# Kernel tuning notes

Hardware: AMD Instinct MI355X
Metric: run time of the kernel (lower is better)

## Reference

```python
import jax, jax.numpy as jnp
import numpy as np

B = 500000
DT = 1.0

def _first_principles_A(dt):
    A = np.eye(8, dtype=np.float32)
    for i in range(4):
        A[i, i + 4] = dt
    return jnp.asarray(A)

def setup_inputs() -> dict:
    key = jax.random.key(0)
    k1, k2 = jax.random.split(key)
    # bbox-like state: keep positions/sizes positive so Q heuristic is sensible
    x = jax.random.uniform(k1, (B, 8, 1), dtype=jnp.float32, minval=0.1, maxval=1.0)
    P = jax.random.normal(k2, (B, 8, 8), dtype=jnp.float32) * 0.1
    A = _first_principles_A(DT)  # relu/triu leave it unchanged but we apply them anyway
    sigma_p = jnp.float32(0.05)
    sigma_v = jnp.float32(0.00625)
    return {"x": x, "P": P, "A": A, "sigma_p": sigma_p, "sigma_v": sigma_v}

def reference(x, P, A, sigma_p, sigma_v):
    # get_motion_matrix: relu then triu
    Ap = jnp.triu(jax.nn.relu(A))  # (8, 8)
    # x_hat = A @ x
    x_hat = jnp.einsum('ij,bjk->bik', Ap, x)  # (B, 8, 1)
    # process-noise heuristic: diag proportional to bbox h, w (x[:,2,0], x[:,3,0])
    h = x[:, 2, 0]
    w = x[:, 3, 0]
    xp, yp = h * sigma_p, w * sigma_p
    xv, yv = h * sigma_v, w * sigma_v
    diag = jnp.stack([xp, yp, xp, yp, xv, yv, xv, yv], axis=-1)  # (B, 8)
    Q = jnp.square(diag)[:, :, None] * jnp.eye(8, dtype=x.dtype)  # (B, 8, 8) diagonal
    # P_hat = A P A^T + Q
    P_hat = jnp.einsum('ij,bjk,lk->bil', Ap, P, Ap) + Q
    return (x_hat, P_hat)
```

## Files before the change

### kernel.cpp

```cpp
#include <hip/hip_runtime.h>


#define ROW_STRIDE 12
#define ELEM_STRIDE 100
#define ELEMS_PER_BLOCK 32

__global__ __launch_bounds__(256) void kalman_predict_kernel(
    const float* __restrict__ x,
    const float* __restrict__ P,
    const float* __restrict__ A,
    const float* __restrict__ sigp_ptr,
    const float* __restrict__ sigv_ptr,
    float* __restrict__ x_hat,
    float* __restrict__ P_hat,
    int B)
{
    __shared__ float lds_m[ELEMS_PER_BLOCK * ELEM_STRIDE];

    float ap[64];
#pragma unroll
    for (int t = 0; t < 64; ++t) {
        float a = fmaxf(A[t], 0.0f);
        if ((t & 7) < (t >> 3)) a = 0.0f;
        ap[t] = __int_as_float(__builtin_amdgcn_readfirstlane(__float_as_int(a)));
    }
    float sigma_p = __int_as_float(__builtin_amdgcn_readfirstlane(__float_as_int(sigp_ptr[0])));
    float sigma_v = __int_as_float(__builtin_amdgcn_readfirstlane(__float_as_int(sigv_ptr[0])));

    int tid = blockIdx.x * blockDim.x + threadIdx.x;
    int e = tid >> 3;
    int r = tid & 7;
    int e_l = threadIdx.x >> 3;

    bool valid = (e < B);
    int e_c = valid ? e : (B - 1);

    const float4* prow = (const float4*)(P + (size_t)e_c * 64 + r * 8);
    float4 pa = prow[0], pb = prow[1];
    float p[8] = {pa.x, pa.y, pa.z, pa.w, pb.x, pb.y, pb.z, pb.w};

    const float4* xrow = (const float4*)(x + (size_t)e_c * 8);
    float4 x0 = xrow[0], x1 = xrow[1];
    float xv[8] = {x0.x, x0.y, x0.z, x0.w, x1.x, x1.y, x1.z, x1.w};

    const float4* arow = (const float4*)(A + r * 8);
    float4 a0 = arow[0], a1 = arow[1];
    float apr[8] = {a0.x, a0.y, a0.z, a0.w, a1.x, a1.y, a1.z, a1.w};
#pragma unroll
    for (int j = 0; j < 8; ++j) {
        float v = fmaxf(apr[j], 0.0f);
        apr[j] = (j >= r) ? v : 0.0f;
    }

    float m[8];
#pragma unroll
    for (int l = 0; l < 8; ++l) {
        float s = 0.0f;
#pragma unroll
        for (int k = 0; k < 8; ++k) s = fmaf(ap[l * 8 + k], p[k], s);
        m[l] = s;
    }

    float* slot = lds_m + e_l * ELEM_STRIDE + r * ROW_STRIDE;
    ((float4*)slot)[0] = make_float4(m[0], m[1], m[2], m[3]);
    ((float4*)(slot + 4))[0] = make_float4(m[4], m[5], m[6], m[7]);

    __syncthreads();

    float hv = (r & 1) ? xv[3] : xv[2];
    float sig = (r < 4) ? sigma_p : sigma_v;
    float q = hv * sig;
    q = q * q;

    float xh = 0.0f;
#pragma unroll
    for (int j = 0; j < 8; ++j) xh = fmaf(apr[j], xv[j], xh);

    float out[8];
#pragma unroll
    for (int l = 0; l < 8; ++l) out[l] = (l == r) ? q : 0.0f;

    const float* ebase = lds_m + e_l * ELEM_STRIDE;
#pragma unroll
    for (int j = 0; j < 8; ++j) {
        const float4* mr = (const float4*)(ebase + j * ROW_STRIDE);
        float4 ma = mr[0], mb = mr[1];
        float mj[8] = {ma.x, ma.y, ma.z, ma.w, mb.x, mb.y, mb.z, mb.w};
#pragma unroll
        for (int l = 0; l < 8; ++l) out[l] = fmaf(apr[j], mj[l], out[l]);
    }

    if (valid) {
        x_hat[(size_t)e * 8 + r] = xh;
        float4* po = (float4*)(P_hat + (size_t)e * 64 + r * 8);
        po[0] = make_float4(out[0], out[1], out[2], out[3]);
        po[1] = make_float4(out[4], out[5], out[6], out[7]);
    }
}

extern "C" void kernel_launch(void* const* d_in, const int* in_sizes, int n_in,
                              void* d_out, int out_size, void* d_ws, size_t ws_size,
                              hipStream_t stream) {
    const float* x  = (const float*)d_in[0];
    const float* P  = (const float*)d_in[1];
    const float* A  = (const float*)d_in[2];
    const float* sp = (const float*)d_in[3];
    const float* sv = (const float*)d_in[4];

    int B = in_sizes[0] / 8;
    float* x_hat = (float*)d_out;
    float* P_hat = (float*)d_out + (size_t)B * 8;

    int threads = B * 8;
    int block = 256;
    int grid = (threads + block - 1) / block;
    kalman_predict_kernel<<<grid, block, 0, stream>>>(x, P, A, sp, sv, x_hat, P_hat, B);
}
```

Before: 253.5 us.

## Precompute masked A in setup kernel, drop block barrier, skip triangular zeros

Adds a tiny setup kernel that applies relu/triu to A and stores it plus sigma values in a global constant buffer, removing per-thread preprocessing from the main kernel. Replaces __syncthreads with a wave-local LDS wait, relying on the 8 threads of each element being in the same wavefront. Skips multiplications by the structurally zero lower triangle and uses 32-bit index arithmetic. Adds a second kernel launch and relies on wavefront-local synchronization assumptions.

Measured after the change: 251.7 us. Within noise of the previous version (-0.7%).

```diff
diff --git a/kernel.cpp b/kernel.cpp
--- a/kernel.cpp
+++ b/kernel.cpp
@@ -5,27 +5,29 @@
 #define ELEM_STRIDE 100
 #define ELEMS_PER_BLOCK 32
 
+__device__ __align__(16) float g_cst[72];
+
+__global__ void kalman_setup_kernel(const float* __restrict__ A,
+                                    const float* __restrict__ sigp_ptr,
+                                    const float* __restrict__ sigv_ptr)
+{
+    int t = threadIdx.x;
+    if (t < 64) {
+        float a = fmaxf(A[t], 0.0f);
+        if ((t & 7) < (t >> 3)) a = 0.0f;
+        g_cst[t] = a;
+    }
+    if (t < 8) g_cst[64 + t] = (t < 4) ? sigp_ptr[0] : sigv_ptr[0];
+}
+
 __global__ __launch_bounds__(256) void kalman_predict_kernel(
     const float* __restrict__ x,
     const float* __restrict__ P,
-    const float* __restrict__ A,
-    const float* __restrict__ sigp_ptr,
-    const float* __restrict__ sigv_ptr,
     float* __restrict__ x_hat,
     float* __restrict__ P_hat,
     int B)
 {
     __shared__ float lds_m[ELEMS_PER_BLOCK * ELEM_STRIDE];
-
-    float ap[64];
-#pragma unroll
-    for (int t = 0; t < 64; ++t) {
-        float a = fmaxf(A[t], 0.0f);
-        if ((t & 7) < (t >> 3)) a = 0.0f;
-        ap[t] = __int_as_float(__builtin_amdgcn_readfirstlane(__float_as_int(a)));
-    }
-    float sigma_p = __int_as_float(__builtin_amdgcn_readfirstlane(__float_as_int(sigp_ptr[0])));
-    float sigma_v = __int_as_float(__builtin_amdgcn_readfirstlane(__float_as_int(sigv_ptr[0])));
 
     int tid = blockIdx.x * blockDim.x + threadIdx.x;
     int e = tid >> 3;
@@ -35,29 +37,31 @@
     bool valid = (e < B);
     int e_c = valid ? e : (B - 1);
 
-    const float4* prow = (const float4*)(P + (size_t)e_c * 64 + r * 8);
+    unsigned poff = (unsigned)e_c * 64u + (unsigned)r * 8u;
+    const float4* prow = (const float4*)(P + poff);
     float4 pa = prow[0], pb = prow[1];
     float p[8] = {pa.x, pa.y, pa.z, pa.w, pb.x, pb.y, pb.z, pb.w};
 
-    const float4* xrow = (const float4*)(x + (size_t)e_c * 8);
+    const float4* xrow = (const float4*)(x + (unsigned)e_c * 8u);
     float4 x0 = xrow[0], x1 = xrow[1];
     float xv[8] = {x0.x, x0.y, x0.z, x0.w, x1.x, x1.y, x1.z, x1.w};
 
-    const float4* arow = (const float4*)(A + r * 8);
+    float ap[64];
+#pragma unroll
+    for (int t = 0; t < 64; ++t) ap[t] = g_cst[t];
+
+    const float4* arow = (const float4*)(g_cst + r * 8);
     float4 a0 = arow[0], a1 = arow[1];
     float apr[8] = {a0.x, a0.y, a0.z, a0.w, a1.x, a1.y, a1.z, a1.w};
-#pragma unroll
-    for (int j = 0; j < 8; ++j) {
-        float v = fmaxf(apr[j], 0.0f);
-        apr[j] = (j >= r) ? v : 0.0f;
-    }
+
+    float sig = g_cst[64 + r];
 
     float m[8];
 #pragma unroll
     for (int l = 0; l < 8; ++l) {
         float s = 0.0f;
 #pragma unroll
-        for (int k = 0; k < 8; ++k) s = fmaf(ap[l * 8 + k], p[k], s);
+        for (int k = l; k < 8; ++k) s = fmaf(ap[l * 8 + k], p[k], s);
         m[l] = s;
     }
 
@@ -65,10 +69,9 @@
     ((float4*)slot)[0] = make_float4(m[0], m[1], m[2], m[3]);
     ((float4*)(slot + 4))[0] = make_float4(m[4], m[5], m[6], m[7]);
 
-    __syncthreads();
+    asm volatile("s_waitcnt lgkmcnt(0)" ::: "memory");
 
     float hv = (r & 1) ? xv[3] : xv[2];
-    float sig = (r < 4) ? sigma_p : sigma_v;
     float q = hv * sig;
     q = q * q;
 
@@ -91,8 +94,8 @@
     }
 
     if (valid) {
-        x_hat[(size_t)e * 8 + r] = xh;
-        float4* po = (float4*)(P_hat + (size_t)e * 64 + r * 8);
+        x_hat[(unsigned)e * 8u + r] = xh;
+        float4* po = (float4*)(P_hat + poff);
         po[0] = make_float4(out[0], out[1], out[2], out[3]);
         po[1] = make_float4(out[4], out[5], out[6], out[7]);
     }
@@ -111,8 +114,10 @@
     float* x_hat = (float*)d_out;
     float* P_hat = (float*)d_out + (size_t)B * 8;
 
+    kalman_setup_kernel<<<1, 64, 0, stream>>>(A, sp, sv);
+
     int threads = B * 8;
     int block = 256;
     int grid = (threads + block - 1) / block;
-    kalman_predict_kernel<<<grid, block, 0, stream>>>(x, P, A, sp, sv, x_hat, P_hat, B);
+    kalman_predict_kernel<<<grid, block, 0, stream>>>(x, P, x_hat, P_hat, B);
 }
```
